# Kernel tuning notes

Measured on AMD Instinct MI355X. Metric: run time of the kernel, lower is better.

Reference implementation:

```python
import jax, jax.numpy as jnp
import numpy as np

B, L, HEADS, D_HEAD = 2, 2048, 16, 64
D_MODEL = HEADS * D_HEAD            # 1024
D_BI = D_MODEL * 4 // 2             # 2048 (bilinear GLU width)
D_PROJ = D_MODEL * 3 + 2 * D_BI
DEPTH = 0                           # block depth < 2 -> token shift active
NEG_INF = -1e10


def _ln(x, g, b, eps=1e-5):
    m = jnp.mean(x, axis=-1, keepdims=True)
    v = jnp.var(x, axis=-1, keepdims=True)
    return (x - m) * jax.lax.rsqrt(v + eps) * g + b


def _shift(x, n):
    # F.pad(x, (0,0,n,-n)): shift along seq dim by n, zero-fill at front
    return jnp.pad(x, ((0, 0), (n, 0), (0, 0)))[:, : x.shape[1], :]


def setup_inputs() -> dict:
    key = jax.random.key(0)
    ks = jax.random.split(key, 3)
    x = jax.random.normal(ks[0], (B, L, D_MODEL), jnp.float32)
    w_in = jax.random.normal(ks[1], (D_MODEL, D_PROJ), jnp.float32) * (D_MODEL ** -0.5)
    # note: torch init zeros out_proj; we use small random weights so backward is non-trivial
    w_out = jax.random.normal(ks[2], (D_MODEL + D_BI, D_MODEL), jnp.float32) * 0.02
    slopes = jnp.concatenate([2.0 ** jnp.linspace(0.0, -6.0, HEADS // 2),
                              jnp.zeros(HEADS - HEADS // 2)]).astype(jnp.float32)
    return {
        "x": x,
        "in_ln_g": jnp.ones(D_MODEL, jnp.float32), "in_ln_b": jnp.zeros(D_MODEL, jnp.float32),
        "mid_ln_g": jnp.ones(D_PROJ, jnp.float32), "mid_ln_b": jnp.zeros(D_PROJ, jnp.float32),
        "out_ln_g": jnp.ones(D_MODEL, jnp.float32), "out_ln_b": jnp.zeros(D_MODEL, jnp.float32),
        "w_in": w_in, "w_out": w_out, "slopes": slopes,
    }


def reference(x, in_ln_g, in_ln_b, mid_ln_g, mid_ln_b, out_ln_g, out_ln_b, w_in, w_out, slopes):
    b, l, d = x.shape
    x = _ln(x, in_ln_g, in_ln_b)
    if DEPTH < 2:
        x = jnp.concatenate([
            _shift(x[..., : d // 4], 1),
            x[..., d // 4: d - d // 8],
            _shift(x[..., d - d // 8:], 2),
        ], axis=-1)
    h = _ln(x @ w_in, mid_ln_g, mid_ln_b)
    q, k, v, p1, p2 = jnp.split(h, [D_MODEL, 2 * D_MODEL, 3 * D_MODEL, 3 * D_MODEL + D_BI], axis=-1)
    to_heads = lambda t: t.reshape(b, l, HEADS, D_HEAD).transpose(0, 2, 1, 3)  # b h l d
    q, k, v = to_heads(q), to_heads(k), to_heads(v)
    logits = jnp.einsum('bhid,bhjd->bhij', q, k) * (D_HEAD ** -0.5)
    pos = jnp.arange(l)
    alibi = pos[None, None, None, :].astype(logits.dtype) * slopes[None, :, None, None]
    causal = jnp.where(pos[:, None] >= pos[None, :], 0.0, NEG_INF).astype(logits.dtype)
    a = jax.nn.softmax(logits + alibi + causal, axis=-1)
    o = jnp.einsum('bhij,bhjd->bhid', a, v).transpose(0, 2, 1, 3).reshape(b, l, d)
    return _ln(jnp.concatenate([o, p1 * p2], axis=-1) @ w_out, out_ln_g, out_ln_b)
```

## Files before the change

kernel.cpp:

```cpp
#include <hip/hip_runtime.h>

#define B_ 2
#define L_ 2048
#define HEADS_ 16
#define DH_ 64
#define DM_ 1024
#define DBI_ 2048
#define DPROJ_ 7168
#define NTOK (B_*L_)
#define DCAT (DM_ + DBI_)

typedef __bf16 bf16;
typedef __attribute__((ext_vector_type(8))) __bf16 bf16x8;
typedef __attribute__((ext_vector_type(4))) __bf16 bf16x4;
typedef __attribute__((ext_vector_type(4))) float floatx4;

typedef __attribute__((address_space(1))) const void gptr_t;
typedef __attribute__((address_space(3))) void lptr_t;

__device__ __forceinline__ void g2l16(const void* g, void* l) {
    __builtin_amdgcn_global_load_lds((gptr_t*)g, (lptr_t*)l, 16, 0, 0);
}

__global__ __launch_bounds__(256) void prep(const float* __restrict__ w_in,
                                            const float* __restrict__ w_out,
                                            bf16* __restrict__ w_inT,
                                            bf16* __restrict__ w_outT,
                                            const float* __restrict__ x,
                                            const float* __restrict__ in_g,
                                            const float* __restrict__ in_b,
                                            bf16* __restrict__ xs) {
    int l = blockIdx.x;
    if (l < 10240) {
        __shared__ float tile[32][33];
        const float* in; bf16* outp; int R, C, bx, by;
        if (l < 7168) { in = w_in;  outp = w_inT;  R = DM_;  C = DPROJ_; bx = l % 224; by = l / 224; }
        else { l -= 7168; in = w_out; outp = w_outT; R = DCAT; C = DM_;   bx = l % 32;  by = l / 32; }
        int c0 = bx * 32, r0 = by * 32;
        int x_ = threadIdx.x & 31, y = threadIdx.x >> 5;
        for (int i = 0; i < 32; i += 8)
            tile[y + i][x_] = in[(size_t)(r0 + y + i) * C + (c0 + x_)];
        __syncthreads();
        for (int i = 0; i < 32; i += 8)
            outp[(size_t)(c0 + y + i) * R + (r0 + x_)] = (bf16)tile[x_][y + i];
        return;
    }
    int tok = l - 10240;
    int b = tok / L_, ll = tok % L_;
    int t = threadIdx.x;
    floatx4 v = *(const floatx4*)(x + (size_t)tok * DM_ + t * 4);
    float s = v[0] + v[1] + v[2] + v[3];
    float s2 = v[0]*v[0] + v[1]*v[1] + v[2]*v[2] + v[3]*v[3];
    __shared__ float red[2][4];
    for (int o = 32; o; o >>= 1) { s += __shfl_xor(s, o); s2 += __shfl_xor(s2, o); }
    int w = t >> 6;
    if ((t & 63) == 0) { red[0][w] = s; red[1][w] = s2; }
    __syncthreads();
    s  = red[0][0] + red[0][1] + red[0][2] + red[0][3];
    s2 = red[1][0] + red[1][1] + red[1][2] + red[1][3];
    float mean = s * (1.f / DM_);
    float var  = s2 * (1.f / DM_) - mean * mean;
    float rstd = rsqrtf(var + 1e-5f);
    int c0 = t * 4;
    floatx4 gg = *(const floatx4*)(in_g + c0);
    floatx4 bv = *(const floatx4*)(in_b + c0);
    bf16x4 y;
    #pragma unroll
    for (int i = 0; i < 4; i++) y[i] = (bf16)((v[i] - mean) * rstd * gg[i] + bv[i]);
    int shift = (c0 < 256) ? 1 : ((c0 >= 896) ? 2 : 0);
    int dl = ll + shift;
    if (dl < L_) *(bf16x4*)(xs + ((size_t)b * L_ + dl) * DM_ + c0) = y;
    if (ll == 0 && shift) {
        bf16x4 z = {};
        *(bf16x4*)(xs + ((size_t)b * L_ + 0) * DM_ + c0) = z;
        if (shift == 2) *(bf16x4*)(xs + ((size_t)b * L_ + 1) * DM_ + c0) = z;
    }
}

__global__ __launch_bounds__(512, 2) void gemm1_fr(const bf16* __restrict__ A,
                                                   const bf16* __restrict__ Bt,
                                                   bf16* __restrict__ C) {
    const int K = DM_, N = DPROJ_;
    int lin = blockIdx.x;
    int xcd = lin & 7, idx = lin >> 3;
    int mt = (xcd >> 2) * 8 + idx / 7;
    int nt = (xcd & 3) * 7 + idx % 7;
    int m0 = mt * 256, n0 = nt * 256;

    __shared__ bf16 As[2][256 * 64];
    __shared__ bf16 Bs[2][256 * 64];

    int t = threadIdx.x;
    int lane = t & 63;
    int c = lane & 15, quad = lane >> 4;
    int wave = t >> 6;
    int wm = (wave >> 2) * 128;
    int wn = (wave & 3) * 64;

    auto stageA = [&](int k0, int bsel, int h) {
        #pragma unroll
        for (int s = 0; s < 2; s++) {
            int g = h * 1024 + s * 512 + t;
            int row = g >> 3;
            int kc = (g & 7) ^ (row & 7);
            g2l16(A + (size_t)(m0 + row) * K + (k0 + kc * 8), &As[bsel][g * 8]);
        }
    };
    auto stageB = [&](int k0, int bsel, int h) {
        #pragma unroll
        for (int s = 0; s < 2; s++) {
            int g = h * 1024 + s * 512 + t;
            int row = g >> 3;
            int kc = (g & 7) ^ (row & 7);
            g2l16(Bt + (size_t)(n0 + row) * K + (k0 + kc * 8), &Bs[bsel][g * 8]);
        }
    };

    floatx4 acc[8][4] = {};

    stageA(0, 0, 0); stageA(0, 0, 1);
    stageB(0, 0, 0); stageB(0, 0, 1);
    stageB(64, 1, 0); stageB(64, 1, 1);
    asm volatile("s_waitcnt vmcnt(4)" ::: "memory");
    __builtin_amdgcn_s_barrier();
    __builtin_amdgcn_sched_barrier(0);

    const int nT = K / 64;
    for (int tt = 0; tt < nT; ++tt) {
        int cur = tt & 1, nxt = cur ^ 1;
        int k1 = (tt + 1) << 6, k2 = (tt + 2) << 6;
        bool dA = (tt + 1 < nT), dB = (tt + 2 < nT);
        bf16x8 bfr[4][2];
        #pragma unroll
        for (int p = 0; p < 4; p++) {
            if      (p == 0) { if (dA) stageA(k1, nxt, 0); }
            else if (p == 1) { if (dA) stageA(k1, nxt, 1); }
            else if (p == 2) { if (dB) stageB(k2, cur, 0); }
            else             { if (dB) stageB(k2, cur, 1); }
            if (p == 0) {
                #pragma unroll
                for (int j = 0; j < 4; j++)
                    #pragma unroll
                    for (int s = 0; s < 2; s++)
                        bfr[j][s] = *(const bf16x8*)&Bs[cur][(wn + j * 16 + c) * 64
                                                            + (((s * 4 + quad) ^ (c & 7)) * 8)];
            }
            bf16x8 af[2][2];
            #pragma unroll
            for (int ii = 0; ii < 2; ii++)
                #pragma unroll
                for (int s = 0; s < 2; s++)
                    af[ii][s] = *(const bf16x8*)&As[cur][(wm + (p * 2 + ii) * 16 + c) * 64
                                                         + (((s * 4 + quad) ^ (c & 7)) * 8)];
            __builtin_amdgcn_s_setprio(1);
            #pragma unroll
            for (int ii = 0; ii < 2; ii++)
                #pragma unroll
                for (int j = 0; j < 4; j++)
                    #pragma unroll
                    for (int s = 0; s < 2; s++)
                        acc[p * 2 + ii][j] = __builtin_amdgcn_mfma_f32_16x16x32_bf16(
                            af[ii][s], bfr[j][s], acc[p * 2 + ii][j], 0, 0, 0);
            __builtin_amdgcn_s_setprio(0);
        }
        asm volatile("s_waitcnt lgkmcnt(0)" ::: "memory");
        if (dB)      { asm volatile("s_waitcnt vmcnt(4)" ::: "memory"); }
        else if (dA) { asm volatile("s_waitcnt vmcnt(0)" ::: "memory"); }
        if (tt + 1 < nT) __builtin_amdgcn_s_barrier();
        __builtin_amdgcn_sched_barrier(0);
    }

    #pragma unroll
    for (int i = 0; i < 8; i++)
        #pragma unroll
        for (int j = 0; j < 4; j++)
            #pragma unroll
            for (int r = 0; r < 4; r++) {
                int row = m0 + wm + i * 16 + quad * 4 + r;
                int col = n0 + wn + j * 16 + c;
                C[(size_t)row * N + col] = (bf16)acc[i][j][r];
            }
}

__global__ __launch_bounds__(512, 1) void gemm2_fr3(const bf16* __restrict__ A,
                                                    const bf16* __restrict__ Bt,
                                                    float* __restrict__ P) {
    const int ldA = DCAT, N = DM_;
    int m0 = blockIdx.x * 128, n0 = blockIdx.y * 256, kz = blockIdx.z;
    const bf16* Ak = A + kz * 1536;
    const bf16* Btk = Bt + kz * 1536;
    float* C = P + (size_t)kz * NTOK * DM_;
    __shared__ bf16 As[2][128 * 64];
    __shared__ bf16 Bs[3][256 * 64];
    int t = threadIdx.x, lane = t & 63, wave = t >> 6;
    int c = lane & 15, quad = lane >> 4;
    int wm = (wave >> 2) * 64;
    int wn = (wave & 3) * 64;

    auto stageA = [&](int k0, int bsel) {
        #pragma unroll
        for (int s = 0; s < 2; s++) {
            int g = s * 512 + t;
            int row = g >> 3;
            int kc = (g & 7) ^ (row & 7);
            g2l16(Ak + (size_t)(m0 + row) * ldA + k0 + kc * 8, &As[bsel][g * 8]);
        }
    };
    auto stageB = [&](int k0, int bsel, int h) {
        #pragma unroll
        for (int s = 0; s < 2; s++) {
            int g = h * 1024 + s * 512 + t;
            int row = g >> 3;
            int kc = (g & 7) ^ (row & 7);
            g2l16(Btk + (size_t)(n0 + row) * ldA + k0 + kc * 8, &Bs[bsel][g * 8]);
        }
    };

    floatx4 acc[4][4] = {};

    stageA(0, 0);
    stageB(0, 0, 0); stageB(0, 0, 1);
    stageB(64, 1, 0); stageB(64, 1, 1);
    asm volatile("s_waitcnt vmcnt(4)" ::: "memory");
    __builtin_amdgcn_s_barrier();
    __builtin_amdgcn_sched_barrier(0);

    const int nT = 1536 / 64;
    int cb = 0, sb = 2;
    for (int tt = 0; tt < nT; ++tt) {
        int ca = tt & 1, na = ca ^ 1;
        int k1 = (tt + 1) << 6, k2 = (tt + 2) << 6;
        bool dA = (tt + 1 < nT), dB = (tt + 2 < nT);
        bf16x8 bfr[4][2];
        #pragma unroll
        for (int p = 0; p < 4; p++) {
            if      (p == 0) { if (dA) stageA(k1, na); }
            else if (p == 1) { if (dB) stageB(k2, sb, 0); }
            else if (p == 2) { if (dB) stageB(k2, sb, 1); }
            if (p == 0) {
                #pragma unroll
                for (int j = 0; j < 4; j++)
                    #pragma unroll
                    for (int s = 0; s < 2; s++)
                        bfr[j][s] = *(const bf16x8*)&Bs[cb][(wn + j * 16 + c) * 64
                                                           + (((s * 4 + quad) ^ (c & 7)) * 8)];
            }
            bf16x8 af[2];
            #pragma unroll
            for (int s = 0; s < 2; s++)
                af[s] = *(const bf16x8*)&As[ca][(wm + p * 16 + c) * 64
                                                + (((s * 4 + quad) ^ (c & 7)) * 8)];
            __builtin_amdgcn_s_setprio(1);
            #pragma unroll
            for (int j = 0; j < 4; j++)
                #pragma unroll
                for (int s = 0; s < 2; s++)
                    acc[p][j] = __builtin_amdgcn_mfma_f32_16x16x32_bf16(
                        af[s], bfr[j][s], acc[p][j], 0, 0, 0);
            __builtin_amdgcn_s_setprio(0);
        }
        asm volatile("s_waitcnt lgkmcnt(0)" ::: "memory");
        if (dB)      { asm volatile("s_waitcnt vmcnt(4)" ::: "memory"); }
        else if (dA) { asm volatile("s_waitcnt vmcnt(0)" ::: "memory"); }
        if (tt + 1 < nT) __builtin_amdgcn_s_barrier();
        __builtin_amdgcn_sched_barrier(0);
        cb = (cb == 2) ? 0 : cb + 1;
        sb = (sb == 2) ? 0 : sb + 1;
    }

    #pragma unroll
    for (int p = 0; p < 4; p++)
        #pragma unroll
        for (int j = 0; j < 4; j++)
            #pragma unroll
            for (int r = 0; r < 4; r++) {
                int row = m0 + wm + p * 16 + quad * 4 + r;
                int col = n0 + wn + j * 16 + c;
                C[(size_t)row * N + col] = acc[p][j][r];
            }
}

__global__ __launch_bounds__(256) void mid_ln_fused(const bf16* __restrict__ h,
                                                    const float* __restrict__ g,
                                                    const float* __restrict__ bb,
                                                    bf16* __restrict__ Qp,
                                                    bf16* __restrict__ Kp,
                                                    bf16* __restrict__ Vn,
                                                    bf16* __restrict__ A2) {
    int tok = blockIdx.x;
    int b = tok >> 11, l = tok & 2047;
    size_t base = (size_t)tok * DPROJ_;
    int t = threadIdx.x;
    float v[28];
    float s = 0.f, s2 = 0.f;
    #pragma unroll
    for (int i = 0; i < 7; i++) {
        bf16x4 r = *(const bf16x4*)(h + base + (size_t)(t + i * 256) * 4);
        #pragma unroll
        for (int k = 0; k < 4; k++) {
            float f = (float)r[k];
            v[i * 4 + k] = f; s += f; s2 += f * f;
        }
    }
    __shared__ float red[2][4];
    for (int o = 32; o; o >>= 1) { s += __shfl_xor(s, o); s2 += __shfl_xor(s2, o); }
    int w = t >> 6;
    if ((t & 63) == 0) { red[0][w] = s; red[1][w] = s2; }
    __syncthreads();
    s  = red[0][0] + red[0][1] + red[0][2] + red[0][3];
    s2 = red[1][0] + red[1][1] + red[1][2] + red[1][3];
    float mean = s * (1.f / DPROJ_);
    float var  = s2 * (1.f / DPROJ_) - mean * mean;
    float rstd = rsqrtf(var + 1e-5f);
    #pragma unroll
    for (int i = 0; i < 7; i++) {
        int C0 = (t + i * 256) * 4;
        floatx4 gg = *(const floatx4*)(g + C0);
        floatx4 bv = *(const floatx4*)(bb + C0);
        #pragma unroll
        for (int k = 0; k < 4; k++)
            v[i * 4 + k] = (v[i * 4 + k] - mean) * rstd * gg[k] + bv[k];
    }
    #pragma unroll
    for (int i = 0; i < 3; i++) {
        int C0 = (t + i * 256) * 4;
        int sec = C0 >> 10, cc = C0 & 1023;
        int hh = cc >> 6, d = cc & 63;
        bf16* dst = (sec == 0) ? Qp : (sec == 1) ? Kp : Vn;
        size_t idx = (((size_t)b * HEADS_ + hh) * L_ + l) * DH_ + d;
        bf16x4 o;
        #pragma unroll
        for (int k = 0; k < 4; k++) o[k] = (bf16)v[i * 4 + k];
        *(bf16x4*)(dst + idx) = o;
    }
    #pragma unroll
    for (int i = 3; i < 5; i++) {
        int off = (t + i * 256) * 4 - 3 * DM_;
        bf16x4 o;
        #pragma unroll
        for (int k = 0; k < 4; k++) o[k] = (bf16)(v[i * 4 + k] * v[(i + 2) * 4 + k]);
        *(bf16x4*)(A2 + (size_t)tok * DCAT + DM_ + off) = o;
    }
}

__global__ __launch_bounds__(256) void vt_pack(const bf16* __restrict__ Vn,
                                               bf16* __restrict__ Vt) {
    __shared__ bf16 tile[32][33];
    int bh = blockIdx.z;
    const bf16* in = Vn + (size_t)bh * L_ * DH_;
    bf16* out = Vt + (size_t)bh * DH_ * L_;
    int l0 = blockIdx.x * 32, d0 = blockIdx.y * 32;
    int x = threadIdx.x & 31, y = threadIdx.x >> 5;
    for (int i = 0; i < 32; i += 8)
        tile[y + i][x] = in[(size_t)(l0 + y + i) * DH_ + d0 + x];
    __syncthreads();
    for (int i = 0; i < 32; i += 8)
        out[(size_t)(d0 + y + i) * L_ + l0 + x] = tile[x][y + i];
}

__global__ __launch_bounds__(256, 4) void attn8(const bf16* __restrict__ Qp,
                                                const bf16* __restrict__ Kp,
                                                const bf16* __restrict__ Vt,
                                                const float* __restrict__ slopes,
                                                bf16* __restrict__ A2) {
    int hd = blockIdx.y, b = blockIdx.z;
    int lin = blockIdx.x + 32 * blockIdx.y + 512 * blockIdx.z;
    int xr = blockIdx.x;
    int qt = ((lin >> 8) & 1) ? (31 - xr) : xr;
    int q0 = qt * 64;
    int t = threadIdx.x, lane = t & 63, wave = t >> 6;
    int quad = lane >> 4, c = lane & 15;
    __shared__ bf16 Ks[2][64 * 64];
    __shared__ bf16 Vs[64 * 64];
    __shared__ bf16 Ps[4][16 * 72];
    int bh = b * HEADS_ + hd;
    const bf16* Qb = Qp + (size_t)bh * L_ * DH_;
    const bf16* Kb = Kp + (size_t)bh * L_ * DH_;
    const bf16* Vb = Vt + (size_t)bh * DH_ * L_;
    const float LOG2E = 1.44269504f;
    float slopeL2 = slopes[hd] * LOG2E;
    const float qscale = 0.125f * LOG2E;

    bf16x8 qf[2];
    int qrow = q0 + wave * 16 + c;
    qf[0] = *(const bf16x8*)(Qb + (size_t)qrow * DH_ + quad * 8);
    qf[1] = *(const bf16x8*)(Qb + (size_t)qrow * DH_ + 32 + quad * 8);
    floatx4 accO[4] = {};
    float lsum[4];
    float mrow[4];
    int i_row0 = q0 + wave * 16 + quad * 4;
    #pragma unroll
    for (int r = 0; r < 4; r++) {
        lsum[r] = 0.f;
        mrow[r] = slopeL2 * (float)(i_row0 + r) + 20.0f;
    }

    auto stageK = [&](int j0, int kb) {
        #pragma unroll
        for (int s = 0; s < 2; s++) {
            int g = s * 256 + t;
            int row = g >> 3;
            int kc = (g & 7) ^ (row & 7);
            g2l16(Kb + (size_t)(j0 + row) * DH_ + kc * 8, &Ks[kb][g * 8]);
        }
    };
    auto stageV = [&](int j0) {
        #pragma unroll
        for (int s = 0; s < 2; s++) {
            int g = s * 256 + t;
            int row = g >> 3;
            int kc = (g & 7) ^ (row & 7);
            g2l16(Vb + (size_t)row * L_ + j0 + kc * 8, &Vs[g * 8]);
        }
    };

    bf16* pw = &Ps[wave][0];
    bf16* pwr = pw + (quad * 4) * 72 + c;

    stageK(0, 0);
    asm volatile("s_waitcnt vmcnt(0)" ::: "memory");
    __builtin_amdgcn_s_barrier();
    __builtin_amdgcn_sched_barrier(0);

    int kb = 0;
    for (int j0 = 0; j0 <= q0; j0 += 64) {
        bool dK = (j0 + 64 <= q0);
        stageV(j0);
        if (dK) stageK(j0 + 64, kb ^ 1);

        bool diag = (j0 == q0);
        #pragma unroll
        for (int nt = 0; nt < 4; nt++) {
            floatx4 sacc = {};
            bf16x8 kf0 = *(const bf16x8*)&Ks[kb][(nt * 16 + c) * 64 + (((0 + quad) ^ (c & 7)) * 8)];
            bf16x8 kf1 = *(const bf16x8*)&Ks[kb][(nt * 16 + c) * 64 + (((4 + quad) ^ (c & 7)) * 8)];
            sacc = __builtin_amdgcn_mfma_f32_16x16x32_bf16(qf[0], kf0, sacc, 0, 0, 0);
            sacc = __builtin_amdgcn_mfma_f32_16x16x32_bf16(qf[1], kf1, sacc, 0, 0, 0);
            int j = j0 + nt * 16 + c;
            float aj = slopeL2 * (float)j;
            #pragma unroll
            for (int r = 0; r < 4; r++) {
                float p = exp2f(fmaf(sacc[r], qscale, aj) - mrow[r]);
                if (diag) p = (j <= i_row0 + r) ? p : 0.f;
                lsum[r] += p;
                pwr[r * 72 + nt * 16] = (bf16)p;
            }
        }
        bf16x8 pf0 = *(const bf16x8*)&pw[c * 72 + quad * 8];
        bf16x8 pf1 = *(const bf16x8*)&pw[c * 72 + 32 + quad * 8];

        if (dK) { asm volatile("s_waitcnt vmcnt(2)" ::: "memory"); }
        else    { asm volatile("s_waitcnt vmcnt(0)" ::: "memory"); }
        __builtin_amdgcn_s_barrier();
        __builtin_amdgcn_sched_barrier(0);

        #pragma unroll
        for (int nt = 0; nt < 4; nt++) {
            bf16x8 vf0 = *(const bf16x8*)&Vs[(nt * 16 + c) * 64 + (((0 + quad) ^ (c & 7)) * 8)];
            bf16x8 vf1 = *(const bf16x8*)&Vs[(nt * 16 + c) * 64 + (((4 + quad) ^ (c & 7)) * 8)];
            accO[nt] = __builtin_amdgcn_mfma_f32_16x16x32_bf16(pf0, vf0, accO[nt], 0, 0, 0);
            accO[nt] = __builtin_amdgcn_mfma_f32_16x16x32_bf16(pf1, vf1, accO[nt], 0, 0, 0);
        }
        asm volatile("s_waitcnt lgkmcnt(0)" ::: "memory");
        __builtin_amdgcn_s_barrier();
        __builtin_amdgcn_sched_barrier(0);
        kb ^= 1;
    }
    #pragma unroll
    for (int r = 0; r < 4; r++) {
        float l = lsum[r];
        l += __shfl_xor(l, 1);
        l += __shfl_xor(l, 2);
        l += __shfl_xor(l, 4);
        l += __shfl_xor(l, 8);
        lsum[r] = 1.f / l;
    }
    #pragma unroll
    for (int r = 0; r < 4; r++) {
        size_t orow = (size_t)b * L_ + q0 + wave * 16 + quad * 4 + r;
        #pragma unroll
        for (int nt = 0; nt < 4; nt++)
            A2[orow * DCAT + hd * DH_ + nt * 16 + c] = (bf16)(accO[nt][r] * lsum[r]);
    }
}

__global__ __launch_bounds__(256) void out_ln2(const float* __restrict__ P,
                                               const float* __restrict__ g,
                                               const float* __restrict__ bb,
                                               float* __restrict__ out) {
    size_t base = (size_t)blockIdx.x * DM_;
    const size_t stride = (size_t)NTOK * DM_;
    int t = threadIdx.x;
    floatx4 a = *(const floatx4*)(P + base + t * 4);
    floatx4 b4 = *(const floatx4*)(P + base + stride + t * 4);
    floatx4 v;
    #pragma unroll
    for (int i = 0; i < 4; i++) v[i] = a[i] + b4[i];
    float s = v[0] + v[1] + v[2] + v[3];
    float s2 = v[0]*v[0] + v[1]*v[1] + v[2]*v[2] + v[3]*v[3];
    __shared__ float red[2][4];
    for (int o = 32; o; o >>= 1) { s += __shfl_xor(s, o); s2 += __shfl_xor(s2, o); }
    int w = t >> 6;
    if ((t & 63) == 0) { red[0][w] = s; red[1][w] = s2; }
    __syncthreads();
    s  = red[0][0] + red[0][1] + red[0][2] + red[0][3];
    s2 = red[1][0] + red[1][1] + red[1][2] + red[1][3];
    float mean = s * (1.f / DM_);
    float var  = s2 * (1.f / DM_) - mean * mean;
    float rstd = rsqrtf(var + 1e-5f);
    int c0 = t * 4;
    floatx4 gg = *(const floatx4*)(g + c0);
    floatx4 bv = *(const floatx4*)(bb + c0);
    floatx4 o;
    #pragma unroll
    for (int i = 0; i < 4; i++) o[i] = (v[i] - mean) * rstd * gg[i] + bv[i];
    *(floatx4*)(out + base + c0) = o;
}

extern "C" void kernel_launch(void* const* d_in, const int* in_sizes, int n_in,
                              void* d_out, int out_size, void* d_ws, size_t ws_size,
                              hipStream_t stream) {
    const float* x     = (const float*)d_in[0];
    const float* in_g  = (const float*)d_in[1];
    const float* in_b  = (const float*)d_in[2];
    const float* mid_g = (const float*)d_in[3];
    const float* mid_b = (const float*)d_in[4];
    const float* out_g = (const float*)d_in[5];
    const float* out_b = (const float*)d_in[6];
    const float* w_in  = (const float*)d_in[7];
    const float* w_out = (const float*)d_in[8];
    const float* slopes = (const float*)d_in[9];
    float* out = (float*)d_out;

    char* ws = (char*)d_ws;
    size_t off = 0;
    auto alloc = [&](size_t n) { char* p = ws + off; off += (n + 255) & ~(size_t)255; return p; };
    bf16* w_inT  = (bf16*)alloc((size_t)DPROJ_ * DM_ * 2);
    bf16* w_outT = (bf16*)alloc((size_t)DM_ * DCAT * 2);
    bf16* xs     = (bf16*)alloc((size_t)NTOK * DM_ * 2);
    bf16* h      = (bf16*)alloc((size_t)NTOK * DPROJ_ * 2);
    bf16* A2     = (bf16*)alloc((size_t)NTOK * DCAT * 2);
    bf16* Qp     = (bf16*)alloc((size_t)NTOK * DM_ * 2);
    bf16* Kp     = (bf16*)alloc((size_t)NTOK * DM_ * 2);
    bf16* Vn     = (bf16*)alloc((size_t)NTOK * DM_ * 2);
    bf16* Vt = xs;
    float* P = (float*)h;

    hipLaunchKernelGGL(prep, dim3(10240 + NTOK), dim3(256), 0, stream,
                       w_in, w_out, w_inT, w_outT, x, in_g, in_b, xs);
    hipLaunchKernelGGL(gemm1_fr, dim3(448), dim3(512), 0, stream, xs, w_inT, h);
    hipLaunchKernelGGL(mid_ln_fused, dim3(NTOK), dim3(256), 0, stream, h, mid_g, mid_b,
                       Qp, Kp, Vn, A2);
    hipLaunchKernelGGL(vt_pack, dim3(L_ / 32, DH_ / 32, B_ * HEADS_), dim3(256), 0, stream, Vn, Vt);
    hipLaunchKernelGGL(attn8, dim3(32, HEADS_, B_), dim3(256), 0, stream, Qp, Kp, Vt, slopes, A2);
    hipLaunchKernelGGL(gemm2_fr3, dim3(NTOK / 128, DM_ / 256, 2), dim3(512), 0, stream,
                       A2, w_outT, P);
    hipLaunchKernelGGL(out_ln2, dim3(NTOK), dim3(256), 0, stream, P, out_g, out_b, out);
}
```

Measured before the change: 295.3 us.

## Retile input GEMM to 256x224 tiles with triple-buffered B and 512 blocks

The input projection GEMM now uses 256x224 output tiles, so the grid is 512 blocks instead of 448 (a multiple of the 256 CUs). The B operand moves to a three-slot ring buffer, and waves are rearranged into a 4x2 layout with 64x112 per-wave tiles. Uneven B staging means the wait counts differ by wave. The aim is better CU balance across waves of blocks and deeper prefetch. The costs are one block per CU (launch bounds 1), more LDS, and more registers for the 28 accumulators and 14 B fragments.

After: 294.5 us. Within noise of the previous version (-0.2%).

```diff
diff --git a/kernel.cpp b/kernel.cpp
--- a/kernel.cpp
+++ b/kernel.cpp
@@ -77,25 +77,25 @@
     }
 }
 
-__global__ __launch_bounds__(512, 2) void gemm1_fr(const bf16* __restrict__ A,
+__global__ __launch_bounds__(512, 1) void gemm1_zt(const bf16* __restrict__ A,
                                                    const bf16* __restrict__ Bt,
                                                    bf16* __restrict__ C) {
     const int K = DM_, N = DPROJ_;
     int lin = blockIdx.x;
     int xcd = lin & 7, idx = lin >> 3;
-    int mt = (xcd >> 2) * 8 + idx / 7;
-    int nt = (xcd & 3) * 7 + idx % 7;
-    int m0 = mt * 256, n0 = nt * 256;
+    int mt = (xcd >> 2) * 8 + (idx >> 3);
+    int nt = (xcd & 3) * 8 + (idx & 7);
+    int m0 = mt * 256, n0 = nt * 224;
 
     __shared__ bf16 As[2][256 * 64];
-    __shared__ bf16 Bs[2][256 * 64];
+    __shared__ bf16 Bs[3][224 * 64];
 
     int t = threadIdx.x;
     int lane = t & 63;
     int c = lane & 15, quad = lane >> 4;
     int wave = t >> 6;
-    int wm = (wave >> 2) * 128;
-    int wn = (wave & 3) * 64;
+    int wm = (wave >> 1) * 64;
+    int wn = (wave & 1) * 112;
 
     auto stageA = [&](int k0, int bsel, int h) {
         #pragma unroll
@@ -106,79 +106,96 @@
             g2l16(A + (size_t)(m0 + row) * K + (k0 + kc * 8), &As[bsel][g * 8]);
         }
     };
-    auto stageB = [&](int k0, int bsel, int h) {
-        #pragma unroll
-        for (int s = 0; s < 2; s++) {
-            int g = h * 1024 + s * 512 + t;
+    auto stageB = [&](int k0, int slot, int h) {
+        if (h == 0) {
+            #pragma unroll
+            for (int s = 0; s < 2; s++) {
+                int g = s * 512 + t;
+                int row = g >> 3;
+                int kc = (g & 7) ^ (row & 7);
+                g2l16(Bt + (size_t)(n0 + row) * K + (k0 + kc * 8), &Bs[slot][g * 8]);
+            }
+        } else {
+            int g = 1024 + t;
             int row = g >> 3;
             int kc = (g & 7) ^ (row & 7);
-            g2l16(Bt + (size_t)(n0 + row) * K + (k0 + kc * 8), &Bs[bsel][g * 8]);
+            g2l16(Bt + (size_t)(n0 + row) * K + (k0 + kc * 8), &Bs[slot][g * 8]);
+            if (wave < 4) {
+                int g2 = 1536 + t;
+                int row2 = g2 >> 3;
+                int kc2 = (g2 & 7) ^ (row2 & 7);
+                g2l16(Bt + (size_t)(n0 + row2) * K + (k0 + kc2 * 8), &Bs[slot][g2 * 8]);
+            }
         }
     };
 
-    floatx4 acc[8][4] = {};
+    floatx4 acc[4][7] = {};
 
     stageA(0, 0, 0); stageA(0, 0, 1);
     stageB(0, 0, 0); stageB(0, 0, 1);
     stageB(64, 1, 0); stageB(64, 1, 1);
-    asm volatile("s_waitcnt vmcnt(4)" ::: "memory");
+    if (wave < 4) { asm volatile("s_waitcnt vmcnt(4)" ::: "memory"); }
+    else          { asm volatile("s_waitcnt vmcnt(3)" ::: "memory"); }
     __builtin_amdgcn_s_barrier();
     __builtin_amdgcn_sched_barrier(0);
 
     const int nT = K / 64;
+    int cb = 0, sb = 2;
     for (int tt = 0; tt < nT; ++tt) {
-        int cur = tt & 1, nxt = cur ^ 1;
+        int ca = tt & 1, na = ca ^ 1;
         int k1 = (tt + 1) << 6, k2 = (tt + 2) << 6;
         bool dA = (tt + 1 < nT), dB = (tt + 2 < nT);
-        bf16x8 bfr[4][2];
+        bf16x8 bfr[7][2];
         #pragma unroll
         for (int p = 0; p < 4; p++) {
-            if      (p == 0) { if (dA) stageA(k1, nxt, 0); }
-            else if (p == 1) { if (dA) stageA(k1, nxt, 1); }
-            else if (p == 2) { if (dB) stageB(k2, cur, 0); }
-            else             { if (dB) stageB(k2, cur, 1); }
+            if      (p == 0) { if (dA) stageA(k1, na, 0); }
+            else if (p == 1) { if (dA) stageA(k1, na, 1); }
+            else if (p == 2) { if (dB) stageB(k2, sb, 0); }
+            else             { if (dB) stageB(k2, sb, 1); }
             if (p == 0) {
                 #pragma unroll
-                for (int j = 0; j < 4; j++)
+                for (int j = 0; j < 7; j++)
                     #pragma unroll
                     for (int s = 0; s < 2; s++)
-                        bfr[j][s] = *(const bf16x8*)&Bs[cur][(wn + j * 16 + c) * 64
-                                                            + (((s * 4 + quad) ^ (c & 7)) * 8)];
-            }
-            bf16x8 af[2][2];
-            #pragma unroll
-            for (int ii = 0; ii < 2; ii++)
+                        bfr[j][s] = *(const bf16x8*)&Bs[cb][(wn + j * 16 + c) * 64
+                                                           + (((s * 4 + quad) ^ (c & 7)) * 8)];
+            }
+            bf16x8 af[2];
+            #pragma unroll
+            for (int s = 0; s < 2; s++)
+                af[s] = *(const bf16x8*)&As[ca][(wm + p * 16 + c) * 64
+                                                + (((s * 4 + quad) ^ (c & 7)) * 8)];
+            __builtin_amdgcn_s_setprio(1);
+            #pragma unroll
+            for (int j = 0; j < 7; j++)
                 #pragma unroll
                 for (int s = 0; s < 2; s++)
-                    af[ii][s] = *(const bf16x8*)&As[cur][(wm + (p * 2 + ii) * 16 + c) * 64
-                                                         + (((s * 4 + quad) ^ (c & 7)) * 8)];
-            __builtin_amdgcn_s_setprio(1);
-            #pragma unroll
-            for (int ii = 0; ii < 2; ii++)
-                #pragma unroll
-                for (int j = 0; j < 4; j++)
-                    #pragma unroll
-                    for (int s = 0; s < 2; s++)
-                        acc[p * 2 + ii][j] = __builtin_amdgcn_mfma_f32_16x16x32_bf16(
-                            af[ii][s], bfr[j][s], acc[p * 2 + ii][j], 0, 0, 0);
+                    acc[p][j] = __builtin_amdgcn_mfma_f32_16x16x32_bf16(
+                        af[s], bfr[j][s], acc[p][j], 0, 0, 0);
             __builtin_amdgcn_s_setprio(0);
         }
         asm volatile("s_waitcnt lgkmcnt(0)" ::: "memory");
-        if (dB)      { asm volatile("s_waitcnt vmcnt(4)" ::: "memory"); }
-        else if (dA) { asm volatile("s_waitcnt vmcnt(0)" ::: "memory"); }
+        if (dB) {
+            if (wave < 4) { asm volatile("s_waitcnt vmcnt(4)" ::: "memory"); }
+            else          { asm volatile("s_waitcnt vmcnt(3)" ::: "memory"); }
+        } else if (dA) {
+            asm volatile("s_waitcnt vmcnt(0)" ::: "memory");
+        }
         if (tt + 1 < nT) __builtin_amdgcn_s_barrier();
         __builtin_amdgcn_sched_barrier(0);
-    }
-
-    #pragma unroll
-    for (int i = 0; i < 8; i++)
-        #pragma unroll
-        for (int j = 0; j < 4; j++)
+        cb = (cb == 2) ? 0 : cb + 1;
+        sb = (sb == 2) ? 0 : sb + 1;
+    }
+
+    #pragma unroll
+    for (int p = 0; p < 4; p++)
+        #pragma unroll
+        for (int j = 0; j < 7; j++)
             #pragma unroll
             for (int r = 0; r < 4; r++) {
-                int row = m0 + wm + i * 16 + quad * 4 + r;
+                int row = m0 + wm + p * 16 + quad * 4 + r;
                 int col = n0 + wn + j * 16 + c;
-                C[(size_t)row * N + col] = (bf16)acc[i][j][r];
+                C[(size_t)row * N + col] = (bf16)acc[p][j][r];
             }
 }
 
@@ -548,7 +565,7 @@
 
     hipLaunchKernelGGL(prep, dim3(10240 + NTOK), dim3(256), 0, stream,
                        w_in, w_out, w_inT, w_outT, x, in_g, in_b, xs);
-    hipLaunchKernelGGL(gemm1_fr, dim3(448), dim3(512), 0, stream, xs, w_inT, h);
+    hipLaunchKernelGGL(gemm1_zt, dim3(512), dim3(512), 0, stream, xs, w_inT, h);
     hipLaunchKernelGGL(mid_ln_fused, dim3(NTOK), dim3(256), 0, stream, h, mid_g, mid_b,
                        Qp, Kp, Vn, A2);
     hipLaunchKernelGGL(vt_pack, dim3(L_ / 32, DH_ / 32, B_ * HEADS_), dim3(256), 0, stream, Vn, Vt);
```

## Shrink gemm1 tiles to 256x128 with K=32 steps for higher occupancy

Applied to the files above, without the earlier changes.

Replaces the 256x256 tile, K=64 gemm1 kernel with a 256x128 tile, K=32 version using a simpler double-buffered loop with __syncthreads, and launches twice as many blocks with launch bounds allowing 4 blocks per CU. The aim is to rely on occupancy to hide latency and spread the grid more evenly across CUs, instead of the hand-tuned staged prefetch and waitcnt schedule. In exchange, data reuse per tile falls, the kernel issues more global and LDS traffic per FLOP, and it synchronises twice as often.

After: 294.7 us. Within noise of the previous version (-0.2%).

```diff
diff --git a/kernel.cpp b/kernel.cpp
--- a/kernel.cpp
+++ b/kernel.cpp
@@ -77,108 +77,85 @@
     }
 }
 
-__global__ __launch_bounds__(512, 2) void gemm1_fr(const bf16* __restrict__ A,
+__global__ __launch_bounds__(512, 4) void gemm1_b2(const bf16* __restrict__ A,
                                                    const bf16* __restrict__ Bt,
                                                    bf16* __restrict__ C) {
     const int K = DM_, N = DPROJ_;
     int lin = blockIdx.x;
     int xcd = lin & 7, idx = lin >> 3;
-    int mt = (xcd >> 2) * 8 + idx / 7;
-    int nt = (xcd & 3) * 7 + idx % 7;
-    int m0 = mt * 256, n0 = nt * 256;
-
-    __shared__ bf16 As[2][256 * 64];
-    __shared__ bf16 Bs[2][256 * 64];
+    int mt = (xcd >> 2) * 8 + idx / 14;
+    int nt = (xcd & 3) * 14 + idx % 14;
+    int m0 = mt * 256, n0 = nt * 128;
+
+    __shared__ bf16 As[2][256 * 32];
+    __shared__ bf16 Bs[2][128 * 32];
 
     int t = threadIdx.x;
     int lane = t & 63;
     int c = lane & 15, quad = lane >> 4;
     int wave = t >> 6;
-    int wm = (wave >> 2) * 128;
-    int wn = (wave & 3) * 64;
-
-    auto stageA = [&](int k0, int bsel, int h) {
+    int wm = (wave >> 1) * 64;
+    int wn = (wave & 1) * 64;
+
+    auto stageA = [&](int k0, int bsel) {
         #pragma unroll
         for (int s = 0; s < 2; s++) {
-            int g = h * 1024 + s * 512 + t;
-            int row = g >> 3;
-            int kc = (g & 7) ^ (row & 7);
+            int g = s * 512 + t;
+            int rp = g >> 3, q = g & 7;
+            int lg = q ^ (rp & 7);
+            int row = rp * 2 + (lg >> 2), kc = lg & 3;
             g2l16(A + (size_t)(m0 + row) * K + (k0 + kc * 8), &As[bsel][g * 8]);
         }
     };
-    auto stageB = [&](int k0, int bsel, int h) {
-        #pragma unroll
-        for (int s = 0; s < 2; s++) {
-            int g = h * 1024 + s * 512 + t;
-            int row = g >> 3;
-            int kc = (g & 7) ^ (row & 7);
-            g2l16(Bt + (size_t)(n0 + row) * K + (k0 + kc * 8), &Bs[bsel][g * 8]);
-        }
-    };
-
-    floatx4 acc[8][4] = {};
-
-    stageA(0, 0, 0); stageA(0, 0, 1);
-    stageB(0, 0, 0); stageB(0, 0, 1);
-    stageB(64, 1, 0); stageB(64, 1, 1);
-    asm volatile("s_waitcnt vmcnt(4)" ::: "memory");
-    __builtin_amdgcn_s_barrier();
-    __builtin_amdgcn_sched_barrier(0);
-
-    const int nT = K / 64;
+    auto stageB = [&](int k0, int bsel) {
+        int g = t;
+        int rp = g >> 3, q = g & 7;
+        int lg = q ^ (rp & 7);
+        int row = rp * 2 + (lg >> 2), kc = lg & 3;
+        g2l16(Bt + (size_t)(n0 + row) * K + (k0 + kc * 8), &Bs[bsel][g * 8]);
+    };
+    auto ldoff = [&](int row, int kc) -> int {
+        int rp = row >> 1;
+        int q = ((row & 1) * 4 + kc) ^ (rp & 7);
+        return (rp * 8 + q) * 8;
+    };
+
+    floatx4 acc[4][4] = {};
+
+    stageA(0, 0); stageB(0, 0);
+    __syncthreads();
+
+    const int nT = K / 32;
+    int buf = 0;
     for (int tt = 0; tt < nT; ++tt) {
-        int cur = tt & 1, nxt = cur ^ 1;
-        int k1 = (tt + 1) << 6, k2 = (tt + 2) << 6;
-        bool dA = (tt + 1 < nT), dB = (tt + 2 < nT);
-        bf16x8 bfr[4][2];
-        #pragma unroll
-        for (int p = 0; p < 4; p++) {
-            if      (p == 0) { if (dA) stageA(k1, nxt, 0); }
-            else if (p == 1) { if (dA) stageA(k1, nxt, 1); }
-            else if (p == 2) { if (dB) stageB(k2, cur, 0); }
-            else             { if (dB) stageB(k2, cur, 1); }
-            if (p == 0) {
-                #pragma unroll
-                for (int j = 0; j < 4; j++)
-                    #pragma unroll
-                    for (int s = 0; s < 2; s++)
-                        bfr[j][s] = *(const bf16x8*)&Bs[cur][(wn + j * 16 + c) * 64
-                                                            + (((s * 4 + quad) ^ (c & 7)) * 8)];
-            }
-            bf16x8 af[2][2];
+        if (tt + 1 < nT) { stageA((tt + 1) << 5, buf ^ 1); stageB((tt + 1) << 5, buf ^ 1); }
+        bf16x8 af[4], bfr[4];
+        #pragma unroll
+        for (int f = 0; f < 4; f++)
+            af[f] = *(const bf16x8*)&As[buf][ldoff(wm + f * 16 + c, quad)];
+        #pragma unroll
+        for (int j = 0; j < 4; j++)
+            bfr[j] = *(const bf16x8*)&Bs[buf][ldoff(wn + j * 16 + c, quad)];
+        __builtin_amdgcn_s_setprio(1);
+        #pragma unroll
+        for (int f = 0; f < 4; f++)
             #pragma unroll
-            for (int ii = 0; ii < 2; ii++)
-                #pragma unroll
-                for (int s = 0; s < 2; s++)
-                    af[ii][s] = *(const bf16x8*)&As[cur][(wm + (p * 2 + ii) * 16 + c) * 64
-                                                         + (((s * 4 + quad) ^ (c & 7)) * 8)];
-            __builtin_amdgcn_s_setprio(1);
-            #pragma unroll
-            for (int ii = 0; ii < 2; ii++)
-                #pragma unroll
-                for (int j = 0; j < 4; j++)
-                    #pragma unroll
-                    for (int s = 0; s < 2; s++)
-                        acc[p * 2 + ii][j] = __builtin_amdgcn_mfma_f32_16x16x32_bf16(
-                            af[ii][s], bfr[j][s], acc[p * 2 + ii][j], 0, 0, 0);
-            __builtin_amdgcn_s_setprio(0);
-        }
-        asm volatile("s_waitcnt lgkmcnt(0)" ::: "memory");
-        if (dB)      { asm volatile("s_waitcnt vmcnt(4)" ::: "memory"); }
-        else if (dA) { asm volatile("s_waitcnt vmcnt(0)" ::: "memory"); }
-        if (tt + 1 < nT) __builtin_amdgcn_s_barrier();
-        __builtin_amdgcn_sched_barrier(0);
-    }
-
-    #pragma unroll
-    for (int i = 0; i < 8; i++)
+            for (int j = 0; j < 4; j++)
+                acc[f][j] = __builtin_amdgcn_mfma_f32_16x16x32_bf16(af[f], bfr[j], acc[f][j], 0, 0, 0);
+        __builtin_amdgcn_s_setprio(0);
+        __syncthreads();
+        buf ^= 1;
+    }
+
+    #pragma unroll
+    for (int f = 0; f < 4; f++)
         #pragma unroll
         for (int j = 0; j < 4; j++)
             #pragma unroll
             for (int r = 0; r < 4; r++) {
-                int row = m0 + wm + i * 16 + quad * 4 + r;
+                int row = m0 + wm + f * 16 + quad * 4 + r;
                 int col = n0 + wn + j * 16 + c;
-                C[(size_t)row * N + col] = (bf16)acc[i][j][r];
+                C[(size_t)row * N + col] = (bf16)acc[f][j][r];
             }
 }
 
@@ -548,7 +525,7 @@
 
     hipLaunchKernelGGL(prep, dim3(10240 + NTOK), dim3(256), 0, stream,
                        w_in, w_out, w_inT, w_outT, x, in_g, in_b, xs);
-    hipLaunchKernelGGL(gemm1_fr, dim3(448), dim3(512), 0, stream, xs, w_inT, h);
+    hipLaunchKernelGGL(gemm1_b2, dim3(896), dim3(512), 0, stream, xs, w_inT, h);
     hipLaunchKernelGGL(mid_ln_fused, dim3(NTOK), dim3(256), 0, stream, h, mid_g, mid_b,
                        Qp, Kp, Vn, A2);
     hipLaunchKernelGGL(vt_pack, dim3(L_ / 32, DH_ / 32, B_ * HEADS_), dim3(256), 0, stream, Vn, Vt);
```
